# Kernel optimization log

Measured on AMD Instinct MI355X. Metric: run time of the kernel, lower is better.

Reference implementation:

```python
import jax, jax.numpy as jnp
import numpy as np

HEAD_SIZE = 64
N_EMBD = 768

def setup_inputs() -> dict:
    key = jax.random.key(0)
    kx, kq, kk, kv = jax.random.split(key, 4)
    x = jax.random.normal(kx, (4, 4096, N_EMBD), dtype=jnp.float32)
    s = 1.0 / np.sqrt(N_EMBD)
    Wq = jax.random.normal(kq, (N_EMBD, HEAD_SIZE), dtype=jnp.float32) * s
    Wk = jax.random.normal(kk, (N_EMBD, HEAD_SIZE), dtype=jnp.float32) * s
    Wv = jax.random.normal(kv, (N_EMBD, HEAD_SIZE), dtype=jnp.float32) * s
    return {"x": x, "Wq": Wq, "Wk": Wk, "Wv": Wv}

def reference(x, Wq, Wk, Wv):
    b, t, c = x.shape
    h = Wq.shape[1]
    q = jnp.einsum('btc,ch->bth', x, Wq)
    k = jnp.einsum('btc,ch->bth', x, Wk)
    v = jnp.einsum('btc,ch->bth', x, Wv)
    scores = jnp.einsum('bqh,bkh->bqk', q, k) / jnp.sqrt(jnp.float32(h))
    causal = jnp.tril(jnp.ones((t, t), dtype=bool))  # [t,t]
    scores = jnp.where(causal, scores, -jnp.inf)
    attn = jax.nn.softmax(scores, axis=-1)
    return jnp.einsum('bqk,bkh->bqh', attn, v)
```

## Files before the change

kernel.cpp:

```cpp
#include <hip/hip_runtime.h>
#include <math.h>

#define BB 4
#define TT 4096
#define CC 768
#define HH 64
#define NN 192
#define LDP 72
#define GR 32
#define BKK 64

typedef __bf16 bf16x8 __attribute__((ext_vector_type(8)));
typedef float floatx4 __attribute__((ext_vector_type(4)));
typedef unsigned short u16x8 __attribute__((ext_vector_type(8)));

__device__ inline unsigned short f2bf(float f) {
    union { __bf16 b; unsigned short u; } v;
    v.b = (__bf16)f;
    return v.u;
}

__global__ __launch_bounds__(256) void wprep(const float* __restrict__ Wq,
                                             const float* __restrict__ Wk,
                                             const float* __restrict__ Wv,
                                             unsigned short* __restrict__ wt) {
    const int idx = blockIdx.x * 256 + threadIdx.x;
    if (idx >= NN * CC) return;
    const int n = idx / CC, c = idx - n * CC;
    const float* W = (n < 64) ? Wq : (n < 128) ? Wk : Wv;
    wt[idx] = f2bf(W[c * HH + (n & 63)]);
}

__global__ __launch_bounds__(256) void qkv_gemm(const float* __restrict__ x,
                                                const unsigned short* __restrict__ wt,
                                                unsigned short* __restrict__ qb,
                                                unsigned short* __restrict__ kb,
                                                unsigned short* __restrict__ vbt) {
    __shared__ unsigned short As[GR * LDP];
    __shared__ unsigned short Bs[NN * LDP];

    const int tid = threadIdx.x;
    const int w = tid >> 6, lane = tid & 63;
    const int l15 = lane & 15, quad = lane >> 4;
    const int m0 = blockIdx.x * GR;
    const int n0 = w * 48;

    floatx4 acc[2][3] = {};

    for (int k0 = 0; k0 < CC; k0 += BKK) {
        __syncthreads();
#pragma unroll
        for (int e = 0; e < 2; ++e) {
            const int c = tid + 256 * e;
            const int r = c >> 4, c4 = (c & 15) * 4;
            const float4 v = *(const float4*)(x + (size_t)(m0 + r) * CC + k0 + c4);
            ushort4 pk;
            pk.x = f2bf(v.x); pk.y = f2bf(v.y); pk.z = f2bf(v.z); pk.w = f2bf(v.w);
            *(ushort4*)(As + r * LDP + c4) = pk;
        }
#pragma unroll
        for (int e = 0; e < 6; ++e) {
            const int c = tid + 256 * e;
            const int r = c >> 3, c8 = (c & 7) * 8;
            *(u16x8*)(Bs + r * LDP + c8) = *(const u16x8*)(wt + (size_t)r * CC + k0 + c8);
        }
        __syncthreads();

        bf16x8 a0[2], a1[2];
#pragma unroll
        for (int rg = 0; rg < 2; ++rg) {
            a0[rg] = *(const bf16x8*)(As + (16 * rg + l15) * LDP + quad * 8);
            a1[rg] = *(const bf16x8*)(As + (16 * rg + l15) * LDP + 32 + quad * 8);
        }
#pragma unroll
        for (int j = 0; j < 3; ++j) {
            const bf16x8 b0 = *(const bf16x8*)(Bs + (n0 + j * 16 + l15) * LDP + quad * 8);
            const bf16x8 b1 = *(const bf16x8*)(Bs + (n0 + j * 16 + l15) * LDP + 32 + quad * 8);
#pragma unroll
            for (int rg = 0; rg < 2; ++rg) {
                acc[rg][j] = __builtin_amdgcn_mfma_f32_16x16x32_bf16(a0[rg], b0, acc[rg][j], 0, 0, 0);
                acc[rg][j] = __builtin_amdgcn_mfma_f32_16x16x32_bf16(a1[rg], b1, acc[rg][j], 0, 0, 0);
            }
        }
    }

    const int b = m0 >> 12;
#pragma unroll
    for (int j = 0; j < 3; ++j) {
        const int n = n0 + j * 16 + l15;
        const int mid = n >> 6;
        const int h = n & 63;
#pragma unroll
        for (int rg = 0; rg < 2; ++rg) {
            const int tloc = (m0 & (TT - 1)) + 16 * rg + quad * 4;
            if (mid == 2) {
                ushort4 pk;
                pk.x = f2bf(acc[rg][j][0]); pk.y = f2bf(acc[rg][j][1]);
                pk.z = f2bf(acc[rg][j][2]); pk.w = f2bf(acc[rg][j][3]);
                *(ushort4*)(vbt + ((size_t)b * HH + h) * TT + tloc) = pk;
            } else {
                unsigned short* dst = (mid == 0) ? qb : kb;
#pragma unroll
                for (int r = 0; r < 4; ++r)
                    dst[(size_t)(m0 + 16 * rg + quad * 4 + r) * HH + h] = f2bf(acc[rg][j][r]);
            }
        }
    }
}

template<int CH>
__global__ __launch_bounds__(256) void attn_part(const unsigned short* __restrict__ qb,
                                                 const unsigned short* __restrict__ kb,
                                                 const unsigned short* __restrict__ vbt,
                                                 float* __restrict__ Opart,
                                                 float* __restrict__ lsum) {
    __shared__ unsigned short Ks[64 * LDP];
    __shared__ unsigned short VTs[64 * LDP];
    __shared__ unsigned short Ps[4][16 * LDP];

    constexpr int NG = 64 / CH;
    constexpr int TOTB = CH * (NG * (NG + 1)) / 2;

    const int b = blockIdx.x & 3;
    int rem = TOTB - 1 - (blockIdx.x >> 2);
    int g = 0;
    while (rem >= CH * (g + 1)) { rem -= CH * (g + 1); ++g; }
    const int qt = g * CH + rem / (g + 1);
    const int ch = rem - (rem / (g + 1)) * (g + 1);

    const int q0  = qt * 64;
    const int tid = threadIdx.x;
    const int w = tid >> 6, lane = tid & 63;
    const int l15 = lane & 15, quad = lane >> 4;

    const unsigned short* Qb  = qb  + (size_t)b * TT * HH;
    const unsigned short* Kb  = kb  + (size_t)b * TT * HH;
    const unsigned short* VTb = vbt + (size_t)b * HH * TT;

    const int qrow = q0 + 16 * w + l15;
    const bf16x8 qf0 = *(const bf16x8*)(Qb + (size_t)qrow * HH + quad * 8);
    const bf16x8 qf1 = *(const bf16x8*)(Qb + (size_t)qrow * HH + 32 + quad * 8);

    floatx4 O[4] = {};
    floatx4 lacc = {0.f, 0.f, 0.f, 0.f};

    const int kt0 = ch * CH;
    const int kt1 = min(kt0 + CH, qt + 1);
    for (int kt = kt0; kt < kt1; ++kt) {
        __syncthreads();
        const unsigned short* Kt = Kb + (size_t)(kt * 64) * HH;
        const unsigned short* Vt = VTb + kt * 64;
#pragma unroll
        for (int e = 0; e < 2; ++e) {
            const int chunk = tid + 256 * e;
            const int r = chunk >> 3, c0 = (chunk & 7) * 8;
            *(u16x8*)(Ks + r * LDP + c0)  = *(const u16x8*)(Kt + r * HH + c0);
            *(u16x8*)(VTs + r * LDP + c0) = *(const u16x8*)(Vt + (size_t)r * TT + c0);
        }
        __syncthreads();

        floatx4 s[4];
#pragma unroll
        for (int ki = 0; ki < 4; ++ki) {
            const bf16x8 kf0 = *(const bf16x8*)(Ks + (16 * ki + l15) * LDP + quad * 8);
            const bf16x8 kf1 = *(const bf16x8*)(Ks + (16 * ki + l15) * LDP + 32 + quad * 8);
            floatx4 c = {};
            c = __builtin_amdgcn_mfma_f32_16x16x32_bf16(qf0, kf0, c, 0, 0, 0);
            c = __builtin_amdgcn_mfma_f32_16x16x32_bf16(qf1, kf1, c, 0, 0, 0);
            s[ki] = c * 0.125f;
        }

        if (kt == qt) {
#pragma unroll
            for (int ki = 0; ki < 4; ++ki)
#pragma unroll
                for (int r = 0; r < 4; ++r) {
                    const int kloc = 16 * ki + l15;
                    const int qloc = 16 * w + quad * 4 + r;
                    if (kloc > qloc) s[ki][r] = -INFINITY;
                }
        }

#pragma unroll
        for (int ki = 0; ki < 4; ++ki)
#pragma unroll
            for (int r = 0; r < 4; ++r) {
                const float p = __expf(s[ki][r]);
                s[ki][r] = p;
                lacc[r] += p;
            }

        unsigned short* Pw = Ps[w];
#pragma unroll
        for (int ki = 0; ki < 4; ++ki)
#pragma unroll
            for (int r = 0; r < 4; ++r)
                Pw[(quad * 4 + r) * LDP + 16 * ki + l15] = f2bf(s[ki][r]);

        const bf16x8 pf0 = *(const bf16x8*)(Pw + l15 * LDP + quad * 8);
        const bf16x8 pf1 = *(const bf16x8*)(Pw + l15 * LDP + 32 + quad * 8);
#pragma unroll
        for (int di = 0; di < 4; ++di) {
            const bf16x8 vf0 = *(const bf16x8*)(VTs + (16 * di + l15) * LDP + quad * 8);
            const bf16x8 vf1 = *(const bf16x8*)(VTs + (16 * di + l15) * LDP + 32 + quad * 8);
            O[di] = __builtin_amdgcn_mfma_f32_16x16x32_bf16(pf0, vf0, O[di], 0, 0, 0);
            O[di] = __builtin_amdgcn_mfma_f32_16x16x32_bf16(pf1, vf1, O[di], 0, 0, 0);
        }
    }

    float l_r[4];
#pragma unroll
    for (int r = 0; r < 4; ++r) {
        float v = lacc[r];
#pragma unroll
        for (int msk = 8; msk >= 1; msk >>= 1) v += __shfl_xor(v, msk, 64);
        l_r[r] = v;
    }

    const int pbase = ((b * 64 + qt) * NG + ch) * 64;
    float* Op = Opart + (size_t)pbase * HH + 16 * w * HH;
#pragma unroll
    for (int di = 0; di < 4; ++di)
#pragma unroll
        for (int r = 0; r < 4; ++r)
            Op[(quad * 4 + r) * HH + 16 * di + l15] = O[di][r];
    if (l15 == 0) {
#pragma unroll
        for (int r = 0; r < 4; ++r)
            lsum[pbase + 16 * w + quad * 4 + r] = l_r[r];
    }
}

template<int CH>
__global__ __launch_bounds__(256) void attn_merge(const float* __restrict__ Opart,
                                                  const float* __restrict__ lsum,
                                                  float* __restrict__ out) {
    constexpr int NG = 64 / CH;
    const int g = blockIdx.x * 256 + threadIdx.x;
    const int row = g >> 6, d = g & 63;
    const int b = row >> 12, t = row & (TT - 1);
    const int qt = t >> 6, rloc = t & 63;
    const int nchunk = qt / CH + 1;
    const int pbase = ((b * 64 + qt) * NG) * 64 + rloc;

    float O = 0.f, L = 0.f;
#pragma unroll 4
    for (int c = 0; c < nchunk; ++c) {
        const int idx = pbase + c * 64;
        L += lsum[idx];
        O += Opart[(size_t)idx * HH + d];
    }
    out[(size_t)row * HH + d] = O / L;
}

__global__ __launch_bounds__(256) void attn_full(const unsigned short* __restrict__ qb,
                                                 const unsigned short* __restrict__ kb,
                                                 const unsigned short* __restrict__ vbt,
                                                 float* __restrict__ out) {
    __shared__ unsigned short Ks[64 * LDP];
    __shared__ unsigned short VTs[64 * LDP];
    __shared__ unsigned short Ps[4][16 * LDP];

    const int b   = blockIdx.x >> 6;
    const int qt  = blockIdx.x & 63;
    const int q0  = qt * 64;
    const int tid = threadIdx.x;
    const int w = tid >> 6, lane = tid & 63;
    const int l15 = lane & 15, quad = lane >> 4;

    const unsigned short* Qb  = qb  + (size_t)b * TT * HH;
    const unsigned short* Kb  = kb  + (size_t)b * TT * HH;
    const unsigned short* VTb = vbt + (size_t)b * HH * TT;

    const int qrow = q0 + 16 * w + l15;
    const bf16x8 qf0 = *(const bf16x8*)(Qb + (size_t)qrow * HH + quad * 8);
    const bf16x8 qf1 = *(const bf16x8*)(Qb + (size_t)qrow * HH + 32 + quad * 8);

    floatx4 O[4] = {};
    floatx4 lacc = {0.f, 0.f, 0.f, 0.f};

    for (int kt = 0; kt <= qt; ++kt) {
        __syncthreads();
        const unsigned short* Kt = Kb + (size_t)(kt * 64) * HH;
        const unsigned short* Vt = VTb + kt * 64;
#pragma unroll
        for (int e = 0; e < 2; ++e) {
            const int chunk = tid + 256 * e;
            const int r = chunk >> 3, c0 = (chunk & 7) * 8;
            *(u16x8*)(Ks + r * LDP + c0)  = *(const u16x8*)(Kt + r * HH + c0);
            *(u16x8*)(VTs + r * LDP + c0) = *(const u16x8*)(Vt + (size_t)r * TT + c0);
        }
        __syncthreads();

        floatx4 s[4];
#pragma unroll
        for (int ki = 0; ki < 4; ++ki) {
            const bf16x8 kf0 = *(const bf16x8*)(Ks + (16 * ki + l15) * LDP + quad * 8);
            const bf16x8 kf1 = *(const bf16x8*)(Ks + (16 * ki + l15) * LDP + 32 + quad * 8);
            floatx4 c = {};
            c = __builtin_amdgcn_mfma_f32_16x16x32_bf16(qf0, kf0, c, 0, 0, 0);
            c = __builtin_amdgcn_mfma_f32_16x16x32_bf16(qf1, kf1, c, 0, 0, 0);
            s[ki] = c * 0.125f;
        }
        if (kt == qt) {
#pragma unroll
            for (int ki = 0; ki < 4; ++ki)
#pragma unroll
                for (int r = 0; r < 4; ++r)
                    if (16 * ki + l15 > 16 * w + quad * 4 + r) s[ki][r] = -INFINITY;
        }
#pragma unroll
        for (int ki = 0; ki < 4; ++ki)
#pragma unroll
            for (int r = 0; r < 4; ++r) {
                const float p = __expf(s[ki][r]);
                s[ki][r] = p; lacc[r] += p;
            }

        unsigned short* Pw = Ps[w];
#pragma unroll
        for (int ki = 0; ki < 4; ++ki)
#pragma unroll
            for (int r = 0; r < 4; ++r)
                Pw[(quad * 4 + r) * LDP + 16 * ki + l15] = f2bf(s[ki][r]);

        const bf16x8 pf0 = *(const bf16x8*)(Pw + l15 * LDP + quad * 8);
        const bf16x8 pf1 = *(const bf16x8*)(Pw + l15 * LDP + 32 + quad * 8);
#pragma unroll
        for (int di = 0; di < 4; ++di) {
            const bf16x8 vf0 = *(const bf16x8*)(VTs + (16 * di + l15) * LDP + quad * 8);
            const bf16x8 vf1 = *(const bf16x8*)(VTs + (16 * di + l15) * LDP + 32 + quad * 8);
            O[di] = __builtin_amdgcn_mfma_f32_16x16x32_bf16(pf0, vf0, O[di], 0, 0, 0);
            O[di] = __builtin_amdgcn_mfma_f32_16x16x32_bf16(pf1, vf1, O[di], 0, 0, 0);
        }
    }
    float l_r[4];
#pragma unroll
    for (int r = 0; r < 4; ++r) {
        float v = lacc[r];
#pragma unroll
        for (int msk = 8; msk >= 1; msk >>= 1) v += __shfl_xor(v, msk, 64);
        l_r[r] = v;
    }
    float* outp = out + ((size_t)b * TT + q0 + 16 * w) * HH;
#pragma unroll
    for (int di = 0; di < 4; ++di)
#pragma unroll
        for (int r = 0; r < 4; ++r)
            outp[(quad * 4 + r) * HH + 16 * di + l15] = O[di][r] / l_r[r];
}

extern "C" void kernel_launch(void* const* d_in, const int* in_sizes, int n_in,
                              void* d_out, int out_size, void* d_ws, size_t ws_size,
                              hipStream_t stream) {
    const float* x  = (const float*)d_in[0];
    const float* Wq = (const float*)d_in[1];
    const float* Wk = (const float*)d_in[2];
    const float* Wv = (const float*)d_in[3];
    float* out = (float*)d_out;

    const size_t nQKV = (size_t)BB * TT * HH;
    unsigned short* qb  = (unsigned short*)d_ws;
    unsigned short* kb  = qb + nQKV;
    unsigned short* vbt = kb + nQKV;
    unsigned short* wt  = vbt + nQKV;
    float* Opart = (float*)(wt + (size_t)NN * CC);

    const size_t prows8  = (size_t)BB * 64 * 8 * 64;
    const size_t prows16 = (size_t)BB * 64 * 4 * 64;
    float* lsum8  = Opart + prows8 * HH;
    float* lsum16 = Opart + prows16 * HH;
    const size_t need8  = (size_t)((char*)(lsum8  + prows8)  - (char*)d_ws);
    const size_t need16 = (size_t)((char*)(lsum16 + prows16) - (char*)d_ws);

    wprep<<<(NN * CC + 255) / 256, 256, 0, stream>>>(Wq, Wk, Wv, wt);
    qkv_gemm<<<(BB * TT) / GR, 256, 0, stream>>>(x, wt, qb, kb, vbt);
    if (ws_size >= need8) {
        attn_part<8><<<BB * 288, 256, 0, stream>>>(qb, kb, vbt, Opart, lsum8);
        attn_merge<8><<<(BB * TT * HH) / 256, 256, 0, stream>>>(Opart, lsum8, out);
    } else if (ws_size >= need16) {
        attn_part<16><<<BB * 160, 256, 0, stream>>>(qb, kb, vbt, Opart, lsum16);
        attn_merge<16><<<(BB * TT * HH) / 256, 256, 0, stream>>>(Opart, lsum16, out);
    } else {
        attn_full<<<BB * (TT / 64), 256, 0, stream>>>(qb, kb, vbt, out);
    }
}
```

Measured before the change: 131.9 us.

## Pre-swizzle weights into MFMA fragment layout and prefetch x tiles into registers

The weight prep kernel now writes W in a fragment-major order that matches the MFMA B-operand lane layout. This lets qkv_gemm load B fragments straight from global memory or L2, which removes the 192x72 shared-memory B tile and its staging stores. The x tile is also register-prefetched one k-step ahead so the global load overlaps the MFMA work. The trade-off is that every wave now re-reads weights from global memory or cache on each step, though the smaller LDS footprint may improve occupancy.

```diff
diff --git a/kernel.cpp b/kernel.cpp
--- a/kernel.cpp
+++ b/kernel.cpp
@@ -23,48 +23,57 @@
 __global__ __launch_bounds__(256) void wprep(const float* __restrict__ Wq,
                                              const float* __restrict__ Wk,
                                              const float* __restrict__ Wv,
-                                             unsigned short* __restrict__ wt) {
+                                             unsigned short* __restrict__ wtf) {
     const int idx = blockIdx.x * 256 + threadIdx.x;
     if (idx >= NN * CC) return;
-    const int n = idx / CC, c = idx - n * CC;
+    const int j = idx & 7;
+    const int lane = (idx >> 3) & 63;
+    const int rest = idx >> 9;
+    const int kg = rest % 24;
+    const int n_tile = rest / 24;
+    const int c = kg * 32 + (lane >> 4) * 8 + j;
+    const int n = n_tile * 16 + (lane & 15);
     const float* W = (n < 64) ? Wq : (n < 128) ? Wk : Wv;
-    wt[idx] = f2bf(W[c * HH + (n & 63)]);
+    wtf[idx] = f2bf(W[c * HH + (n & 63)]);
 }
 
 __global__ __launch_bounds__(256) void qkv_gemm(const float* __restrict__ x,
-                                                const unsigned short* __restrict__ wt,
+                                                const unsigned short* __restrict__ wtf,
                                                 unsigned short* __restrict__ qb,
                                                 unsigned short* __restrict__ kb,
                                                 unsigned short* __restrict__ vbt) {
     __shared__ unsigned short As[GR * LDP];
-    __shared__ unsigned short Bs[NN * LDP];
 
     const int tid = threadIdx.x;
     const int w = tid >> 6, lane = tid & 63;
     const int l15 = lane & 15, quad = lane >> 4;
     const int m0 = blockIdx.x * GR;
     const int n0 = w * 48;
+    const int nt0 = w * 3;
+
+    const int ar = tid >> 3;
+    const int akoff = (tid & 7) * 8;
+    const float* xp = x + (size_t)(m0 + ar) * CC + akoff;
 
     floatx4 acc[2][3] = {};
 
-    for (int k0 = 0; k0 < CC; k0 += BKK) {
-        __syncthreads();
-#pragma unroll
-        for (int e = 0; e < 2; ++e) {
-            const int c = tid + 256 * e;
-            const int r = c >> 4, c4 = (c & 15) * 4;
-            const float4 v = *(const float4*)(x + (size_t)(m0 + r) * CC + k0 + c4);
-            ushort4 pk;
-            pk.x = f2bf(v.x); pk.y = f2bf(v.y); pk.z = f2bf(v.z); pk.w = f2bf(v.w);
-            *(ushort4*)(As + r * LDP + c4) = pk;
-        }
-#pragma unroll
-        for (int e = 0; e < 6; ++e) {
-            const int c = tid + 256 * e;
-            const int r = c >> 3, c8 = (c & 7) * 8;
-            *(u16x8*)(Bs + r * LDP + c8) = *(const u16x8*)(wt + (size_t)r * CC + k0 + c8);
-        }
-        __syncthreads();
+    float4 pa0 = *(const float4*)(xp);
+    float4 pa1 = *(const float4*)(xp + 4);
+
+    for (int step = 0; step < 12; ++step) {
+        __syncthreads();
+        u16x8 pk;
+        pk[0] = f2bf(pa0.x); pk[1] = f2bf(pa0.y);
+        pk[2] = f2bf(pa0.z); pk[3] = f2bf(pa0.w);
+        pk[4] = f2bf(pa1.x); pk[5] = f2bf(pa1.y);
+        pk[6] = f2bf(pa1.z); pk[7] = f2bf(pa1.w);
+        *(u16x8*)(As + ar * LDP + akoff) = pk;
+        __syncthreads();
+
+        if (step < 11) {
+            pa0 = *(const float4*)(xp + (step + 1) * BKK);
+            pa1 = *(const float4*)(xp + (step + 1) * BKK + 4);
+        }
 
         bf16x8 a0[2], a1[2];
 #pragma unroll
@@ -74,8 +83,10 @@
         }
 #pragma unroll
         for (int j = 0; j < 3; ++j) {
-            const bf16x8 b0 = *(const bf16x8*)(Bs + (n0 + j * 16 + l15) * LDP + quad * 8);
-            const bf16x8 b1 = *(const bf16x8*)(Bs + (n0 + j * 16 + l15) * LDP + 32 + quad * 8);
+            const unsigned short* bp =
+                wtf + ((size_t)((nt0 + j) * 24 + 2 * step) * 64 + lane) * 8;
+            const bf16x8 b0 = *(const bf16x8*)(bp);
+            const bf16x8 b1 = *(const bf16x8*)(bp + 512);
 #pragma unroll
             for (int rg = 0; rg < 2; ++rg) {
                 acc[rg][j] = __builtin_amdgcn_mfma_f32_16x16x32_bf16(a0[rg], b0, acc[rg][j], 0, 0, 0);
@@ -363,8 +374,8 @@
     unsigned short* qb  = (unsigned short*)d_ws;
     unsigned short* kb  = qb + nQKV;
     unsigned short* vbt = kb + nQKV;
-    unsigned short* wt  = vbt + nQKV;
-    float* Opart = (float*)(wt + (size_t)NN * CC);
+    unsigned short* wtf = vbt + nQKV;
+    float* Opart = (float*)(wtf + (size_t)NN * CC);
 
     const size_t prows8  = (size_t)BB * 64 * 8 * 64;
     const size_t prows16 = (size_t)BB * 64 * 4 * 64;
@@ -373,8 +384,8 @@
     const size_t need8  = (size_t)((char*)(lsum8  + prows8)  - (char*)d_ws);
     const size_t need16 = (size_t)((char*)(lsum16 + prows16) - (char*)d_ws);
 
-    wprep<<<(NN * CC + 255) / 256, 256, 0, stream>>>(Wq, Wk, Wv, wt);
-    qkv_gemm<<<(BB * TT) / GR, 256, 0, stream>>>(x, wt, qb, kb, vbt);
+    wprep<<<(NN * CC + 255) / 256, 256, 0, stream>>>(Wq, Wk, Wv, wtf);
+    qkv_gemm<<<(BB * TT) / GR, 256, 0, stream>>>(x, wtf, qb, kb, vbt);
     if (ws_size >= need8) {
         attn_part<8><<<BB * 288, 256, 0, stream>>>(qb, kb, vbt, Opart, lsum8);
         attn_merge<8><<<(BB * TT * HH) / 256, 256, 0, stream>>>(Opart, lsum8, out);
```

New measurement: 131.9 us. About the same (+0.0%).
